# Kernel tuning notes

Hardware: AMD Instinct MI355X
Metric: run time of the kernel (lower is better)

## Reference

```python
import jax, jax.numpy as jnp
import numpy as np

N_NODES = 50000
N_EDGES = 800000
D = 64
N_REL = 16


def setup_inputs() -> dict:
    key = jax.random.key(0)
    ks = jax.random.split(key, 8)
    return {
        "nfeat": jax.random.normal(ks[0], (N_NODES, D), dtype=jnp.float32),
        "efeat": jax.random.normal(ks[1], (N_EDGES, D), dtype=jnp.float32),
        "relation_W": jax.random.normal(ks[2], (N_REL, D, D), dtype=jnp.float32) * (1.0 / np.sqrt(D)),
        "W1": jax.random.normal(ks[3], (D, D), dtype=jnp.float32) * (1.0 / np.sqrt(D)),
        "W2": jax.random.normal(ks[4], (D, D), dtype=jnp.float32) * (1.0 / np.sqrt(D)),
        "src": jax.random.randint(ks[5], (N_EDGES,), 0, N_NODES, dtype=jnp.int32),
        "dst": jax.random.randint(ks[6], (N_EDGES,), 0, N_NODES, dtype=jnp.int32),
        "etype": jax.random.randint(ks[7], (N_EDGES,), 0, N_REL, dtype=jnp.int32),
    }


def _leaky_relu(x, slope=0.01):
    return jnp.where(x >= 0, x, slope * x)


def reference(nfeat, efeat, relation_W, W1, W2, src, dst, etype):
    N, Din = nfeat.shape
    R, _, Dr = relation_W.shape
    # W_r h for every (relation, node) pair, then gather per-edge.
    # Mathematically identical to per-edge bmm_maybe_select, but avoids the
    # (E, Din, Dr) per-edge weight materialization.
    proj = jnp.einsum('nd,rde->rne', nfeat, relation_W).reshape(R * N, Dr)  # (R*N, Dr)
    flat_src = etype * N + src
    flat_dst = etype * N + dst
    t_r = proj[flat_src]  # (E, Dr) == W_r h_t
    h_r = proj[flat_dst]  # (E, Dr) == W_r h_h
    # att = (W_r h_t)^T tanh(W_r h_h + e_r)
    att = jnp.sum(t_r * jnp.tanh(h_r + efeat), axis=-1)  # (E,)
    # edge softmax grouped by destination node
    seg_max = jax.ops.segment_max(att, dst, num_segments=N)  # (N,)
    ex = jnp.exp(att - seg_max[dst])
    denom = jax.ops.segment_sum(ex, dst, num_segments=N)  # (N,)
    a = ex / denom[dst]  # (E,)
    # u_mul_e + sum scatter aggregation
    h_neighbor = jax.ops.segment_sum(nfeat[src] * a[:, None], dst, num_segments=N)  # (N, Din)
    # Bi-interaction residual
    out = _leaky_relu((nfeat + h_neighbor) @ W1) + _leaky_relu((nfeat * h_neighbor) @ W2)
    return (h_neighbor, out)
```

## Files before the change

kernel.cpp:

```cpp
#include <hip/hip_runtime.h>
#include <math.h>


#define DIM 64
#define PA 72

typedef _Float16 half8 __attribute__((ext_vector_type(8)));
typedef float f32x4 __attribute__((ext_vector_type(4)));
typedef unsigned int u32x4 __attribute__((ext_vector_type(4)));

__device__ __forceinline__ float4 f4zero() { return make_float4(0.f, 0.f, 0.f, 0.f); }

__device__ __forceinline__ unsigned short f2bf(float x) {
    unsigned u = __float_as_uint(x);
    u += 0x7FFFu + ((u >> 16) & 1u);
    return (unsigned short)(u >> 16);
}

__device__ __forceinline__ float fast_tanh(float x) {
    float ex = __expf(2.0f * x);
    return 1.0f - 2.0f / (ex + 1.0f);
}

__device__ __forceinline__ void bf8up(u32x4 u, float* f) {
    f[0] = __uint_as_float(u[0] << 16);
    f[1] = __uint_as_float(u[0] & 0xFFFF0000u);
    f[2] = __uint_as_float(u[1] << 16);
    f[3] = __uint_as_float(u[1] & 0xFFFF0000u);
    f[4] = __uint_as_float(u[2] << 16);
    f[5] = __uint_as_float(u[2] & 0xFFFF0000u);
    f[6] = __uint_as_float(u[3] << 16);
    f[7] = __uint_as_float(u[3] & 0xFFFF0000u);
}

__global__ __launch_bounds__(256) void k_proj(const float* __restrict__ nfeat,
                                              const float* __restrict__ relW,
                                              unsigned short* __restrict__ proj,
                                              int N, int R) {
    __shared__ _Float16 shA[64 * PA];
    __shared__ _Float16 shB[64 * PA];
    unsigned short* shSt = (unsigned short*)shA;

    const int tx = threadIdx.x;
    const int n0 = blockIdx.x * 64;

    const float4* nf4 = (const float4*)(nfeat + (size_t)n0 * DIM);
#pragma unroll
    for (int i = 0; i < 4; ++i) {
        int idx = tx + 256 * i;
        int row = idx >> 4, c = idx & 15;
        float4 v = (n0 + row < N) ? nf4[idx] : f4zero();
        _Float16* p = &shA[row * PA + c * 4];
        p[0] = (_Float16)v.x; p[1] = (_Float16)v.y;
        p[2] = (_Float16)v.z; p[3] = (_Float16)v.w;
    }
    __syncthreads();

    const int w = tx >> 6;
    const int lane = tx & 63;
    const int lm = lane & 15;
    const int lq = lane >> 4;
    const int m0 = w * 16;

    half8 a0 = *(const half8*)&shA[(m0 + lm) * PA + 0 * 32 + lq * 8];
    half8 a1 = *(const half8*)&shA[(m0 + lm) * PA + 1 * 32 + lq * 8];

    for (int r = 0; r < R; ++r) {
        __syncthreads();
        const float4* Wr4 = (const float4*)(relW + (size_t)r * DIM * DIM);
#pragma unroll
        for (int i = 0; i < 4; ++i) {
            int idx = tx + 256 * i;
            int d = idx >> 4, c = (idx & 15) * 4;
            float4 v = Wr4[idx];
            shB[(c + 0) * PA + d] = (_Float16)v.x;
            shB[(c + 1) * PA + d] = (_Float16)v.y;
            shB[(c + 2) * PA + d] = (_Float16)v.z;
            shB[(c + 3) * PA + d] = (_Float16)v.w;
        }
        __syncthreads();

        f32x4 acc[4];
#pragma unroll
        for (int ct = 0; ct < 4; ++ct) {
            half8 b0 = *(const half8*)&shB[(ct * 16 + lm) * PA + 0 * 32 + lq * 8];
            half8 b1 = *(const half8*)&shB[(ct * 16 + lm) * PA + 1 * 32 + lq * 8];
            f32x4 c = {0.f, 0.f, 0.f, 0.f};
            c = __builtin_amdgcn_mfma_f32_16x16x32_f16(a0, b0, c, 0, 0, 0);
            c = __builtin_amdgcn_mfma_f32_16x16x32_f16(a1, b1, c, 0, 0, 0);
            acc[ct] = c;
        }

#pragma unroll
        for (int ct = 0; ct < 4; ++ct) {
#pragma unroll
            for (int i = 0; i < 4; ++i) {
                int row = m0 + lq * 4 + i;
                int col = ct * 16 + lm;
                shSt[row * PA + col] = f2bf(acc[ct][i]);
            }
        }
        __syncthreads();

        unsigned short* projR = proj + ((size_t)r * N + n0) * DIM;
#pragma unroll
        for (int k = 0; k < 2; ++k) {
            int chunk = tx + k * 256;
            int row = chunk >> 3, cc = chunk & 7;
            uint4 v = *(const uint4*)&shSt[row * PA + cc * 8];
            if (n0 + row < N)
                *(uint4*)&projR[(size_t)row * DIM + cc * 8] = v;
        }
    }
}

__global__ __launch_bounds__(256) void k_hist(const int* __restrict__ dst,
                                              int* __restrict__ deg,
                                              int* __restrict__ rank, int E) {
    int e = blockIdx.x * 256 + threadIdx.x;
    if (e < E) rank[e] = atomicAdd(&deg[dst[e]], 1);
}

__global__ __launch_bounds__(256) void k_scan1(const int* __restrict__ deg,
                                               int* __restrict__ epart,
                                               int* __restrict__ bsum, int N) {
    __shared__ int sh[256];
    int i = blockIdx.x * 256 + threadIdx.x;
    int t = threadIdx.x;
    int v = (i < N) ? deg[i] : 0;
    sh[t] = v;
    __syncthreads();
#pragma unroll
    for (int d = 1; d < 256; d <<= 1) {
        int o = (t >= d) ? sh[t - d] : 0;
        __syncthreads();
        sh[t] += o;
        __syncthreads();
    }
    if (i < N) epart[i] = sh[t] - v;
    if (t == 255) bsum[blockIdx.x] = sh[255];
}

__global__ __launch_bounds__(1024) void k_scan2(const int* __restrict__ epart,
                                                const int* __restrict__ bsum,
                                                int nb,
                                                int* __restrict__ off,
                                                int N, int E) {
    __shared__ int bx[256];
    int t = threadIdx.x;
    int v = 0;
    if (t < 256) {
        v = (t < nb) ? bsum[t] : 0;
        bx[t] = v;
    }
    __syncthreads();
#pragma unroll
    for (int d = 1; d < 256; d <<= 1) {
        int o = 0;
        if (t < 256 && t >= d) o = bx[t - d];
        __syncthreads();
        if (t < 256) bx[t] += o;
        __syncthreads();
    }
    if (t < 256) bx[t] -= v;
    __syncthreads();
    for (int i = t; i < N; i += 1024)
        off[i] = epart[i] + bx[i >> 8];
    if (t == 0) off[N] = E;
}

__global__ __launch_bounds__(256) void k_att(const unsigned short* __restrict__ proj,
                                             const float* __restrict__ efeat,
                                             const int* __restrict__ src,
                                             const int* __restrict__ dst,
                                             const int* __restrict__ etype,
                                             const int* __restrict__ rank,
                                             const int* __restrict__ off,
                                             float* __restrict__ att_s,
                                             int* __restrict__ src_s,
                                             int N, int E) {
    int t = blockIdx.x * 256 + threadIdx.x;
    int e = t >> 3;
    int sub = t & 7;
    if (e >= E) return;
    int s = src[e], d = dst[e], r = etype[e];

    const u32x4* tp = (const u32x4*)(proj + ((size_t)((unsigned)(r * N + s))) * DIM) + sub;
    const u32x4* hp = (const u32x4*)(proj + ((size_t)((unsigned)(r * N + d))) * DIM) + sub;
    const f32x4* ef = (const f32x4*)(efeat + (size_t)e * DIM) + sub * 2;

    u32x4 tu = *tp;
    u32x4 hu = *hp;
    f32x4 efa = __builtin_nontemporal_load(ef);
    f32x4 efb = __builtin_nontemporal_load(ef + 1);

    float tf[8], hf[8];
    bf8up(tu, tf);
    bf8up(hu, hf);
    float ev[8] = {efa[0], efa[1], efa[2], efa[3], efb[0], efb[1], efb[2], efb[3]};

    float dotv = 0.f;
#pragma unroll
    for (int i = 0; i < 8; ++i)
        dotv = fmaf(tf[i], fast_tanh(hf[i] + ev[i]), dotv);

    dotv += __shfl_xor(dotv, 1);
    dotv += __shfl_xor(dotv, 2);
    dotv += __shfl_xor(dotv, 4);

    int p = off[d] + rank[e];
    if (sub == 0) att_s[p] = dotv;
    if (sub == 1) src_s[p] = s;
}

__global__ __launch_bounds__(256) void k_aggB(const float* __restrict__ att_s,
                                              const int* __restrict__ src_s,
                                              const float* __restrict__ nfeat,
                                              const int* __restrict__ off,
                                              const float* __restrict__ W1,
                                              const float* __restrict__ W2,
                                              float* __restrict__ hn,
                                              float* __restrict__ out,
                                              int N) {
    __shared__ float shW[2][DIM * DIM];
    const int tx = threadIdx.x;
    {
        const float4* w14 = (const float4*)W1;
        const float4* w24 = (const float4*)W2;
        float4* s0 = (float4*)shW[0];
        float4* s1 = (float4*)shW[1];
#pragma unroll
        for (int i = 0; i < 4; ++i) {
            s0[tx + 256 * i] = w14[tx + 256 * i];
            s1[tx + 256 * i] = w24[tx + 256 * i];
        }
    }
    __syncthreads();

    const int node = blockIdx.x * 4 + (tx >> 6);
    if (node >= N) return;
    const int lane = tx & 63;

    const int jb = off[node];
    const int je = off[node + 1];

    float m = -INFINITY;
    for (int j0 = jb; j0 < je; j0 += 64) {
        int j = j0 + lane;
        float a = (j < je) ? att_s[j] : -INFINITY;
        m = fmaxf(m, a);
    }
#pragma unroll
    for (int ms = 32; ms; ms >>= 1) m = fmaxf(m, __shfl_xor(m, ms));

    float pl = 0.f, acc = 0.f, acc2 = 0.f;
    for (int j0 = jb; j0 < je; j0 += 64) {
        int j = j0 + lane;
        int cnt = min(64, je - j0);
        float a = (j < je) ? att_s[j] : -INFINITY;
        float p = __expf(a - m);
        int s = (j < je) ? src_s[j] : 0;
        pl += p;
        int jj = 0;
        for (; jj + 3 < cnt; jj += 4) {
            float pj0 = __shfl(p, jj + 0);
            float pj1 = __shfl(p, jj + 1);
            float pj2 = __shfl(p, jj + 2);
            float pj3 = __shfl(p, jj + 3);
            int sj0 = __shfl(s, jj + 0);
            int sj1 = __shfl(s, jj + 1);
            int sj2 = __shfl(s, jj + 2);
            int sj3 = __shfl(s, jj + 3);
            float x0 = nfeat[(size_t)sj0 * DIM + lane];
            float x1 = nfeat[(size_t)sj1 * DIM + lane];
            float x2 = nfeat[(size_t)sj2 * DIM + lane];
            float x3 = nfeat[(size_t)sj3 * DIM + lane];
            acc  = fmaf(pj0, x0, acc);
            acc2 = fmaf(pj1, x1, acc2);
            acc  = fmaf(pj2, x2, acc);
            acc2 = fmaf(pj3, x3, acc2);
        }
        for (; jj < cnt; ++jj) {
            float pj = __shfl(p, jj);
            int sj = __shfl(s, jj);
            acc = fmaf(pj, nfeat[(size_t)sj * DIM + lane], acc);
        }
    }
    acc += acc2;
#pragma unroll
    for (int ms = 32; ms; ms >>= 1) pl += __shfl_xor(pl, ms);

    const float hval = (je > jb) ? acc / pl : 0.f;
    hn[(size_t)node * DIM + lane] = hval;

    const float nf = nfeat[(size_t)node * DIM + lane];
    const float v1 = nf + hval;
    const float v2 = nf * hval;
    float o1 = 0.f, o2 = 0.f;
#pragma unroll 8
    for (int d = 0; d < DIM; ++d) {
        float s1 = __shfl(v1, d);
        float s2 = __shfl(v2, d);
        o1 = fmaf(s1, shW[0][d * DIM + lane], o1);
        o2 = fmaf(s2, shW[1][d * DIM + lane], o2);
    }
    out[(size_t)node * DIM + lane] =
        (o1 >= 0.f ? o1 : 0.01f * o1) + (o2 >= 0.f ? o2 : 0.01f * o2);
}

extern "C" void kernel_launch(void* const* d_in, const int* in_sizes, int n_in,
                              void* d_out, int out_size, void* d_ws, size_t ws_size,
                              hipStream_t stream) {
    const float* nfeat = (const float*)d_in[0];
    const float* efeat = (const float*)d_in[1];
    const float* relW  = (const float*)d_in[2];
    const float* W1    = (const float*)d_in[3];
    const float* W2    = (const float*)d_in[4];
    const int* src   = (const int*)d_in[5];
    const int* dst   = (const int*)d_in[6];
    const int* etype = (const int*)d_in[7];

    const int N = in_sizes[0] / DIM;
    const int E = in_sizes[5];
    const int R = in_sizes[2] / (DIM * DIM);
    const int NB = (N + 255) / 256;

    float* out = (float*)d_out;
    float* hn  = out;
    float* bi  = out + (size_t)N * DIM;

    unsigned short* proj = (unsigned short*)d_ws;
    size_t projElems = (size_t)R * N * DIM;
    int* deg    = (int*)(proj + projElems);
    int* off    = deg + N;
    int* epart  = off + (N + 1);
    int* bsum   = epart + N;
    int* rank   = bsum + 256;
    int* src_s  = rank + E;
    float* att_s = (float*)(src_s + E);

    (void)hipMemsetAsync(deg, 0, (size_t)N * sizeof(int), stream);

    k_hist<<<(E + 255) / 256, 256, 0, stream>>>(dst, deg, rank, E);
    k_scan1<<<NB, 256, 0, stream>>>(deg, epart, bsum, N);
    k_scan2<<<1, 1024, 0, stream>>>(epart, bsum, NB, off, N, E);

    k_proj<<<(N + 63) / 64, 256, 0, stream>>>(nfeat, relW, proj, N, R);

    k_att<<<((size_t)E * 8 + 255) / 256, 256, 0, stream>>>(proj, efeat, src, dst, etype,
                                                           rank, off, att_s, src_s, N, E);

    k_aggB<<<(N + 3) / 4, 256, 0, stream>>>(att_s, src_s, nfeat, off,
                                            W1, W2, hn, bi, N);
}
```

Measured before the change: 568.2 us.

## Split aggregation and bi-interaction kernels, use MFMA for output GEMMs, split projection grid

The fused aggregation kernel is split in two. k_agg does only the softmax-weighted neighbour gather, now with an 8-way unrolled gather and four accumulators. A new k_bi kernel computes both bi-interaction 64x64 GEMMs with fp16 MFMA, replacing the scalar shuffle-based FMA loop and freeing the aggregation kernel of its 32KB of shared memory, which should help occupancy. k_proj's relation loop is also split across two grid-y blocks for more parallelism. The cost is an extra launch, an extra pass over hn, and fp16 rounding in the output GEMMs. R is assumed even.

```diff
diff --git a/kernel.cpp b/kernel.cpp
--- a/kernel.cpp
+++ b/kernel.cpp
@@ -43,6 +43,8 @@
 
     const int tx = threadIdx.x;
     const int n0 = blockIdx.x * 64;
+    const int rpb = R >> 1;
+    const int rb = blockIdx.y * rpb;
 
     const float4* nf4 = (const float4*)(nfeat + (size_t)n0 * DIM);
 #pragma unroll
@@ -65,7 +67,8 @@
     half8 a0 = *(const half8*)&shA[(m0 + lm) * PA + 0 * 32 + lq * 8];
     half8 a1 = *(const half8*)&shA[(m0 + lm) * PA + 1 * 32 + lq * 8];
 
-    for (int r = 0; r < R; ++r) {
+    for (int rr = 0; rr < rpb; ++rr) {
+        const int r = rb + rr;
         __syncthreads();
         const float4* Wr4 = (const float4*)(relW + (size_t)r * DIM * DIM);
 #pragma unroll
@@ -213,33 +216,14 @@
     if (sub == 1) src_s[p] = s;
 }
 
-__global__ __launch_bounds__(256) void k_aggB(const float* __restrict__ att_s,
-                                              const int* __restrict__ src_s,
-                                              const float* __restrict__ nfeat,
-                                              const int* __restrict__ off,
-                                              const float* __restrict__ W1,
-                                              const float* __restrict__ W2,
-                                              float* __restrict__ hn,
-                                              float* __restrict__ out,
-                                              int N) {
-    __shared__ float shW[2][DIM * DIM];
-    const int tx = threadIdx.x;
-    {
-        const float4* w14 = (const float4*)W1;
-        const float4* w24 = (const float4*)W2;
-        float4* s0 = (float4*)shW[0];
-        float4* s1 = (float4*)shW[1];
-#pragma unroll
-        for (int i = 0; i < 4; ++i) {
-            s0[tx + 256 * i] = w14[tx + 256 * i];
-            s1[tx + 256 * i] = w24[tx + 256 * i];
-        }
-    }
-    __syncthreads();
-
-    const int node = blockIdx.x * 4 + (tx >> 6);
+__global__ __launch_bounds__(256) void k_agg(const float* __restrict__ att_s,
+                                             const int* __restrict__ src_s,
+                                             const float* __restrict__ nfeat,
+                                             const int* __restrict__ off,
+                                             float* __restrict__ hn, int N) {
+    const int node = blockIdx.x * 4 + (threadIdx.x >> 6);
     if (node >= N) return;
-    const int lane = tx & 63;
+    const int lane = threadIdx.x & 63;
 
     const int jb = off[node];
     const int je = off[node + 1];
@@ -253,7 +237,8 @@
 #pragma unroll
     for (int ms = 32; ms; ms >>= 1) m = fmaxf(m, __shfl_xor(m, ms));
 
-    float pl = 0.f, acc = 0.f, acc2 = 0.f;
+    float pl = 0.f;
+    float ac0 = 0.f, ac1 = 0.f, ac2 = 0.f, ac3 = 0.f;
     for (int j0 = jb; j0 < je; j0 += 64) {
         int j = j0 + lane;
         int cnt = min(64, je - j0);
@@ -262,50 +247,137 @@
         int s = (j < je) ? src_s[j] : 0;
         pl += p;
         int jj = 0;
-        for (; jj + 3 < cnt; jj += 4) {
-            float pj0 = __shfl(p, jj + 0);
-            float pj1 = __shfl(p, jj + 1);
-            float pj2 = __shfl(p, jj + 2);
-            float pj3 = __shfl(p, jj + 3);
-            int sj0 = __shfl(s, jj + 0);
-            int sj1 = __shfl(s, jj + 1);
-            int sj2 = __shfl(s, jj + 2);
-            int sj3 = __shfl(s, jj + 3);
-            float x0 = nfeat[(size_t)sj0 * DIM + lane];
-            float x1 = nfeat[(size_t)sj1 * DIM + lane];
-            float x2 = nfeat[(size_t)sj2 * DIM + lane];
-            float x3 = nfeat[(size_t)sj3 * DIM + lane];
-            acc  = fmaf(pj0, x0, acc);
-            acc2 = fmaf(pj1, x1, acc2);
-            acc  = fmaf(pj2, x2, acc);
-            acc2 = fmaf(pj3, x3, acc2);
+        for (; jj + 7 < cnt; jj += 8) {
+            float pj[8]; int sj[8]; float x[8];
+#pragma unroll
+            for (int u = 0; u < 8; ++u) {
+                pj[u] = __shfl(p, jj + u);
+                sj[u] = __shfl(s, jj + u);
+            }
+#pragma unroll
+            for (int u = 0; u < 8; ++u)
+                x[u] = nfeat[(size_t)sj[u] * DIM + lane];
+            ac0 = fmaf(pj[0], x[0], ac0);
+            ac1 = fmaf(pj[1], x[1], ac1);
+            ac2 = fmaf(pj[2], x[2], ac2);
+            ac3 = fmaf(pj[3], x[3], ac3);
+            ac0 = fmaf(pj[4], x[4], ac0);
+            ac1 = fmaf(pj[5], x[5], ac1);
+            ac2 = fmaf(pj[6], x[6], ac2);
+            ac3 = fmaf(pj[7], x[7], ac3);
         }
         for (; jj < cnt; ++jj) {
             float pj = __shfl(p, jj);
             int sj = __shfl(s, jj);
-            acc = fmaf(pj, nfeat[(size_t)sj * DIM + lane], acc);
-        }
-    }
-    acc += acc2;
+            ac0 = fmaf(pj, nfeat[(size_t)sj * DIM + lane], ac0);
+        }
+    }
+    float acc = (ac0 + ac1) + (ac2 + ac3);
 #pragma unroll
     for (int ms = 32; ms; ms >>= 1) pl += __shfl_xor(pl, ms);
 
     const float hval = (je > jb) ? acc / pl : 0.f;
     hn[(size_t)node * DIM + lane] = hval;
-
-    const float nf = nfeat[(size_t)node * DIM + lane];
-    const float v1 = nf + hval;
-    const float v2 = nf * hval;
-    float o1 = 0.f, o2 = 0.f;
-#pragma unroll 8
-    for (int d = 0; d < DIM; ++d) {
-        float s1 = __shfl(v1, d);
-        float s2 = __shfl(v2, d);
-        o1 = fmaf(s1, shW[0][d * DIM + lane], o1);
-        o2 = fmaf(s2, shW[1][d * DIM + lane], o2);
-    }
-    out[(size_t)node * DIM + lane] =
-        (o1 >= 0.f ? o1 : 0.01f * o1) + (o2 >= 0.f ? o2 : 0.01f * o2);
+}
+
+__global__ __launch_bounds__(256) void k_bi(const float* __restrict__ nfeat,
+                                            const float* __restrict__ hn,
+                                            const float* __restrict__ W1,
+                                            const float* __restrict__ W2,
+                                            float* __restrict__ out, int N) {
+    __shared__ _Float16 shA1[64 * PA];
+    __shared__ _Float16 shA2[64 * PA];
+    __shared__ _Float16 shB1[64 * PA];
+    __shared__ _Float16 shB2[64 * PA];
+
+    const int tx = threadIdx.x;
+    const int n0 = blockIdx.x * 64;
+
+    const float4* nf4 = (const float4*)(nfeat + (size_t)n0 * DIM);
+    const float4* hn4 = (const float4*)(hn + (size_t)n0 * DIM);
+#pragma unroll
+    for (int i = 0; i < 4; ++i) {
+        int idx = tx + 256 * i;
+        int row = idx >> 4, c = idx & 15;
+        bool ok = (n0 + row < N);
+        float4 a = ok ? nf4[idx] : f4zero();
+        float4 b = ok ? hn4[idx] : f4zero();
+        _Float16* p1 = &shA1[row * PA + c * 4];
+        _Float16* p2 = &shA2[row * PA + c * 4];
+        p1[0] = (_Float16)(a.x + b.x); p2[0] = (_Float16)(a.x * b.x);
+        p1[1] = (_Float16)(a.y + b.y); p2[1] = (_Float16)(a.y * b.y);
+        p1[2] = (_Float16)(a.z + b.z); p2[2] = (_Float16)(a.z * b.z);
+        p1[3] = (_Float16)(a.w + b.w); p2[3] = (_Float16)(a.w * b.w);
+    }
+    const float4* w14 = (const float4*)W1;
+    const float4* w24 = (const float4*)W2;
+#pragma unroll
+    for (int i = 0; i < 4; ++i) {
+        int idx = tx + 256 * i;
+        int k = idx >> 4, c = (idx & 15) * 4;
+        float4 v = w14[idx];
+        shB1[(c + 0) * PA + k] = (_Float16)v.x;
+        shB1[(c + 1) * PA + k] = (_Float16)v.y;
+        shB1[(c + 2) * PA + k] = (_Float16)v.z;
+        shB1[(c + 3) * PA + k] = (_Float16)v.w;
+        float4 u = w24[idx];
+        shB2[(c + 0) * PA + k] = (_Float16)u.x;
+        shB2[(c + 1) * PA + k] = (_Float16)u.y;
+        shB2[(c + 2) * PA + k] = (_Float16)u.z;
+        shB2[(c + 3) * PA + k] = (_Float16)u.w;
+    }
+    __syncthreads();
+
+    const int w = tx >> 6;
+    const int lane = tx & 63;
+    const int lm = lane & 15;
+    const int lq = lane >> 4;
+    const int m0 = w * 16;
+
+    half8 a10 = *(const half8*)&shA1[(m0 + lm) * PA + 0 * 32 + lq * 8];
+    half8 a11 = *(const half8*)&shA1[(m0 + lm) * PA + 1 * 32 + lq * 8];
+    half8 a20 = *(const half8*)&shA2[(m0 + lm) * PA + 0 * 32 + lq * 8];
+    half8 a21 = *(const half8*)&shA2[(m0 + lm) * PA + 1 * 32 + lq * 8];
+
+    f32x4 res[4];
+#pragma unroll
+    for (int ct = 0; ct < 4; ++ct) {
+        half8 b10 = *(const half8*)&shB1[(ct * 16 + lm) * PA + 0 * 32 + lq * 8];
+        half8 b11 = *(const half8*)&shB1[(ct * 16 + lm) * PA + 1 * 32 + lq * 8];
+        half8 b20 = *(const half8*)&shB2[(ct * 16 + lm) * PA + 0 * 32 + lq * 8];
+        half8 b21 = *(const half8*)&shB2[(ct * 16 + lm) * PA + 1 * 32 + lq * 8];
+        f32x4 c1 = {0.f, 0.f, 0.f, 0.f};
+        f32x4 c2 = {0.f, 0.f, 0.f, 0.f};
+        c1 = __builtin_amdgcn_mfma_f32_16x16x32_f16(a10, b10, c1, 0, 0, 0);
+        c1 = __builtin_amdgcn_mfma_f32_16x16x32_f16(a11, b11, c1, 0, 0, 0);
+        c2 = __builtin_amdgcn_mfma_f32_16x16x32_f16(a20, b20, c2, 0, 0, 0);
+        c2 = __builtin_amdgcn_mfma_f32_16x16x32_f16(a21, b21, c2, 0, 0, 0);
+#pragma unroll
+        for (int i = 0; i < 4; ++i) {
+            float o1 = c1[i], o2 = c2[i];
+            res[ct][i] = (o1 >= 0.f ? o1 : 0.01f * o1) + (o2 >= 0.f ? o2 : 0.01f * o2);
+        }
+    }
+
+    __syncthreads();
+    float* shSt = (float*)shA1;
+#pragma unroll
+    for (int ct = 0; ct < 4; ++ct)
+#pragma unroll
+        for (int i = 0; i < 4; ++i)
+            shSt[(m0 + lq * 4 + i) * 68 + ct * 16 + lm] = res[ct][i];
+    __syncthreads();
+
+    float* outp = out + (size_t)n0 * DIM;
+#pragma unroll
+    for (int k = 0; k < 4; ++k) {
+        int idx = tx + 256 * k;
+        int row = idx >> 4, cc = idx & 15;
+        if (n0 + row < N) {
+            float4 v = *(const float4*)&shSt[row * 68 + cc * 4];
+            *(float4*)&outp[(size_t)row * DIM + cc * 4] = v;
+        }
+    }
 }
 
 extern "C" void kernel_launch(void* const* d_in, const int* in_sizes, int n_in,
@@ -345,11 +417,13 @@
     k_scan1<<<NB, 256, 0, stream>>>(deg, epart, bsum, N);
     k_scan2<<<1, 1024, 0, stream>>>(epart, bsum, NB, off, N, E);
 
-    k_proj<<<(N + 63) / 64, 256, 0, stream>>>(nfeat, relW, proj, N, R);
+    dim3 gProj((N + 63) / 64, 2);
+    k_proj<<<gProj, 256, 0, stream>>>(nfeat, relW, proj, N, R);
 
     k_att<<<((size_t)E * 8 + 255) / 256, 256, 0, stream>>>(proj, efeat, src, dst, etype,
                                                            rank, off, att_s, src_s, N, E);
 
-    k_aggB<<<(N + 3) / 4, 256, 0, stream>>>(att_s, src_s, nfeat, off,
-                                            W1, W2, hn, bi, N);
-}
+    k_agg<<<(N + 3) / 4, 256, 0, stream>>>(att_s, src_s, nfeat, off, hn, N);
+
+    k_bi<<<(N + 63) / 64, 256, 0, stream>>>(nfeat, hn, W1, W2, bi, N);
+}
```

Measured after the change: 474.6 us. 16.5% less time.
